# Kernel optimization log

Hardware: AMD Instinct MI355X
Metric: run time of the kernel (lower is better)

## Reference

```python
import jax, jax.numpy as jnp
import numpy as np

N_NODES, N_EDGES, F_IN, HID, N_CLASSES = 50000, 800000, 128, 128, 10
HEADS, D_HEAD, N_GRAPHS, N_CONV = 4, 32, 256, 3
BN_EPS = 1e-5
NEG_SLOPE = 0.2


def batchnorm(x, g, b):
    # training-mode BN: batch mean / biased variance over dim 0
    m = x.mean(axis=0)
    v = x.var(axis=0)
    return (x - m) * jax.lax.rsqrt(v + BN_EPS) * g + b


def segment_softmax(logits, seg, n):
    # numerically stable softmax over edges grouped by destination node
    m = jax.ops.segment_max(logits, seg, num_segments=n)
    e = jnp.exp(logits - m[seg])
    s = jax.ops.segment_sum(e, seg, num_segments=n)
    return e / (s[seg] + 1e-16)


def gat_conv(x, src, dst, W, a_src, a_dst, bias):
    # PyG GATConv (concat=True), eval mode (no attention dropout)
    n = x.shape[0]
    h = (x @ W).reshape(n, HEADS, D_HEAD)                 # [N,H,Dh]
    al_s = jnp.einsum('nhd,hd->nh', h, a_src)             # alpha from source
    al_d = jnp.einsum('nhd,hd->nh', h, a_dst)             # alpha from dest
    logits = jax.nn.leaky_relu(al_s[src] + al_d[dst], NEG_SLOPE)   # [E,H]
    alpha = segment_softmax(logits, dst, n)                # softmax over incoming edges
    msg = h[src] * alpha[:, :, None]                       # [E,H,Dh]
    out = jax.ops.segment_sum(msg, dst, num_segments=n)    # [N,H,Dh]
    return out.reshape(n, HEADS * D_HEAD) + bias


def setup_inputs() -> dict:
    key = jax.random.key(0)
    ks = jax.random.split(key, 12)
    s = 0.05
    inp = {
        'x': jax.random.normal(ks[0], (N_NODES, F_IN), dtype=jnp.float32),
        'edge_index': jax.random.randint(ks[1], (2, N_EDGES), 0, N_NODES, dtype=jnp.int32),
        'batch': jnp.sort(jax.random.randint(ks[2], (N_NODES,), 0, N_GRAPHS, dtype=jnp.int32)),
        # GCNConv(gfn=True): plain weight, no bias used
        'w_feat': s * jax.random.normal(ks[3], (F_IN, HID), dtype=jnp.float32),
        'bnf_g': jnp.ones((F_IN,), jnp.float32),
        'bnf_b': jnp.full((F_IN,), 1e-4, jnp.float32),
        'bnc_g': jnp.ones((N_CONV, HID), jnp.float32),
        'bnc_b': jnp.full((N_CONV, HID), 1e-4, jnp.float32),
        'gat_w': s * jax.random.normal(ks[4], (N_CONV, HID, HID), dtype=jnp.float32),
        'gat_asrc': s * jax.random.normal(ks[5], (N_CONV, HEADS, D_HEAD), dtype=jnp.float32),
        'gat_adst': s * jax.random.normal(ks[6], (N_CONV, HEADS, D_HEAD), dtype=jnp.float32),
        'gat_b': jnp.zeros((N_CONV, HID), jnp.float32),
        'bnfc_g': jnp.ones((HID,), jnp.float32),
        'bnfc_b': jnp.full((HID,), 1e-4, jnp.float32),
        'lin_w': s * jax.random.normal(ks[7], (HID, HID), dtype=jnp.float32),
        'lin_b': jnp.zeros((HID,), jnp.float32),
        'bnh_g': jnp.ones((HID,), jnp.float32),
        'bnh_b': jnp.full((HID,), 1e-4, jnp.float32),
        'cls_w': s * jax.random.normal(ks[8], (HID, N_CLASSES), dtype=jnp.float32),
        'cls_b': jnp.zeros((N_CLASSES,), jnp.float32),
    }
    return inp


def reference(x, edge_index, batch, w_feat, bnf_g, bnf_b, bnc_g, bnc_b,
              gat_w, gat_asrc, gat_adst, gat_b, bnfc_g, bnfc_b,
              lin_w, lin_b, bnh_g, bnh_b, cls_w, cls_b):
    n = x.shape[0]
    loops = jnp.arange(n, dtype=edge_index.dtype)
    src = jnp.concatenate([edge_index[0], loops])   # self-loops (PyG GATConv default)
    dst = jnp.concatenate([edge_index[1], loops])

    h = jax.nn.relu(batchnorm(x, bnf_g, bnf_b) @ w_feat)   # bn_feat + gfn GCNConv + relu
    for i in range(N_CONV):
        h = batchnorm(h, bnc_g[i], bnc_b[i])
        h = jax.nn.relu(gat_conv(h, src, dst, gat_w[i], gat_asrc[i], gat_adst[i], gat_b[i]))

    g = jax.ops.segment_sum(h, batch, num_segments=N_GRAPHS)   # global_add_pool [G,HID]
    g = jax.nn.relu(batchnorm(g, bnfc_g, bnfc_b) @ lin_w + lin_b)
    g = batchnorm(g, bnh_g, bnh_b)
    # dropout inactive in eval mode
    return jax.nn.log_softmax(g @ cls_w + cls_b, axis=-1)
```

## Files before the change

kernel.cpp:

```cpp
#include <hip/hip_runtime.h>
#include <math.h>

#define N_NODES 50000
#define N_EDGES 800000
#define NGRAPHS 256
#define NCONV 3
#define SCAT_CHUNK 2048
#define DMAX 64

typedef _Float16 h4 __attribute__((ext_vector_type(4)));
typedef _Float16 h8 __attribute__((ext_vector_type(8)));
typedef float f32x4 __attribute__((ext_vector_type(4)));

static inline int divup(int a, int b) { return (a + b - 1) / b; }

#define SB_CONV 0
#define SB_H1 2048
#define SB_H2 2304
#define SB_X 2560

__global__ void init_kernel(float* __restrict__ SB, int* __restrict__ cursor,
                            int* __restrict__ col, int n) {
    int i = blockIdx.x * blockDim.x + threadIdx.x;
    if (i < 2816) SB[i] = 0.f;
    if (i < n) {
        cursor[i] = 1;
        col[(size_t)i * DMAX] = i;
    }
}

__global__ __launch_bounds__(256) void scatter_edges_xcd(const int* __restrict__ src,
                                                         const int* __restrict__ dst,
                                                         int* __restrict__ cursor,
                                                         int* __restrict__ col, int E) {
    int slice = blockIdx.x & 7;
    int base = (blockIdx.x >> 3) * SCAT_CHUNK;
    int lim = min(base + SCAT_CHUNK, E);
    int lo = slice * (N_NODES / 8);
    int hi = lo + (N_NODES / 8);
    for (int i = base + threadIdx.x; i < lim; i += 256) {
        int d = dst[i];
        if (d >= lo && d < hi) {
            int p = atomicAdd(&cursor[d], 1);
            if (p < DMAX) col[(size_t)d * DMAX + p] = src[i];
        }
    }
}

__global__ __launch_bounds__(256) void cast_stats(const float* __restrict__ x,
                                                  _Float16* __restrict__ y, int n,
                                                  float* __restrict__ sums) {
    __shared__ float S[16][128], S2[16][128];
    int tid = threadIdx.x;
    int c8 = (tid & 15) * 8;
    int rg = tid >> 4;
    float s[8] = {}, s2[8] = {};
    for (int r = blockIdx.x * 16 + rg; r < n; r += gridDim.x * 16) {
        const float4* p = (const float4*)&x[(size_t)r * 128 + c8];
        float4 v0 = p[0], v1 = p[1];
        float f[8] = {v0.x, v0.y, v0.z, v0.w, v1.x, v1.y, v1.z, v1.w};
        h8 o;
#pragma unroll
        for (int i = 0; i < 8; ++i) {
            o[i] = (_Float16)f[i];
            s[i] += f[i];
            s2[i] += f[i] * f[i];
        }
        *(h8*)&y[(size_t)r * 128 + c8] = o;
    }
#pragma unroll
    for (int i = 0; i < 8; ++i) { S[rg][c8 + i] = s[i]; S2[rg][c8 + i] = s2[i]; }
    __syncthreads();
    if (tid < 128) {
        float a = 0.f, b = 0.f;
#pragma unroll
        for (int k = 0; k < 16; ++k) { a += S[k][tid]; b += S2[k][tid]; }
        atomicAdd(&sums[tid], a);
        atomicAdd(&sums[128 + tid], b);
    }
}

__global__ __launch_bounds__(256) void colstats_h(const _Float16* __restrict__ x, int n,
                                                  float* __restrict__ sums) {
    __shared__ float S[16][128], S2[16][128];
    int tid = threadIdx.x;
    int c8 = (tid & 15) * 8;
    int rg = tid >> 4;
    float s[8] = {}, s2[8] = {};
    for (int r = blockIdx.x * 16 + rg; r < n; r += gridDim.x * 16) {
        h8 v = *(const h8*)&x[(size_t)r * 128 + c8];
#pragma unroll
        for (int i = 0; i < 8; ++i) {
            float f = (float)v[i];
            s[i] += f;
            s2[i] += f * f;
        }
    }
#pragma unroll
    for (int i = 0; i < 8; ++i) { S[rg][c8 + i] = s[i]; S2[rg][c8 + i] = s2[i]; }
    __syncthreads();
    if (tid < 128) {
        float a = 0.f, b = 0.f;
#pragma unroll
        for (int k = 0; k < 16; ++k) { a += S[k][tid]; b += S2[k][tid]; }
        atomicAdd(&sums[tid], a);
        atomicAdd(&sums[128 + tid], b);
    }
}

__global__ __launch_bounds__(256) void colstats_small16(const float* __restrict__ x, int rows,
                                                        float* __restrict__ sums) {
    __shared__ float S[16][128], S2[16][128];
    int tid = threadIdx.x;
    int c8 = (tid & 15) * 8;
    int rg = tid >> 4;
    float s[8] = {}, s2[8] = {};
    for (int r = blockIdx.x * 16 + rg; r < rows; r += gridDim.x * 16) {
        const float4* p = (const float4*)&x[(size_t)r * 128 + c8];
        float4 v0 = p[0], v1 = p[1];
        float f[8] = {v0.x, v0.y, v0.z, v0.w, v1.x, v1.y, v1.z, v1.w};
#pragma unroll
        for (int i = 0; i < 8; ++i) { s[i] += f[i]; s2[i] += f[i] * f[i]; }
    }
#pragma unroll
    for (int i = 0; i < 8; ++i) { S[rg][c8 + i] = s[i]; S2[rg][c8 + i] = s2[i]; }
    __syncthreads();
    if (tid < 128) {
        float a = 0.f, b = 0.f;
#pragma unroll
        for (int k = 0; k < 16; ++k) { a += S[k][tid]; b += S2[k][tid]; }
        atomicAdd(&sums[tid], a);
        atomicAdd(&sums[128 + tid], b);
    }
}

__global__ __launch_bounds__(128) void fold_t(const float* __restrict__ sums, int nsl,
                                              float inv_n,
                                              const float* __restrict__ gamma,
                                              const float* __restrict__ beta,
                                              const float* __restrict__ W,
                                              _Float16* __restrict__ WTh, float* __restrict__ bp) {
    int j = blockIdx.x, k = threadIdx.x;
    float s1 = 0.f, s2v = 0.f;
    for (int s = 0; s < nsl; ++s) { s1 += sums[s * 256 + k]; s2v += sums[s * 256 + 128 + k]; }
    float mean = s1 * inv_n;
    float var = s2v * inv_n - mean * mean;
    float sc = gamma[k] * rsqrtf(var + 1e-5f);
    float t = beta[k] - mean * sc;
    float w = W[k * 128 + j];
    WTh[j * 128 + k] = (_Float16)(sc * w);
    float pb = t * w;
    for (int off = 1; off < 64; off <<= 1) pb += __shfl_xor(pb, off, 64);
    __shared__ float r2[2];
    if ((k & 63) == 0) r2[k >> 6] = pb;
    __syncthreads();
    if (k == 0) bp[j] = r2[0] + r2[1];
}

__global__ __launch_bounds__(256) void gemm_mfma(const _Float16* __restrict__ Ah,
                                                 const _Float16* __restrict__ WTh,
                                                 const float* __restrict__ bp,
                                                 _Float16* __restrict__ outh, int n, int relu,
                                                 const float* __restrict__ asrc,
                                                 const float* __restrict__ adst,
                                                 float* __restrict__ als,
                                                 float* __restrict__ ald,
                                                 float* __restrict__ stats8,
                                                 float* __restrict__ sums_zero) {
    __shared__ _Float16 Wl[128 * 136];
    __shared__ float SSm[4 * 128], SS2m[4 * 128];
    int tid = threadIdx.x;
    if (sums_zero && blockIdx.x < 8) sums_zero[blockIdx.x * 256 + tid] = 0.f;
    for (int i = tid; i < 2048; i += 256) {
        int r = i >> 4, s = i & 15;
        *(h8*)&Wl[r * 136 + s * 8] = *(const h8*)&WTh[r * 128 + s * 8];
    }
    __syncthreads();
    int lane = tid & 63, wid = tid >> 6;
    int m = lane & 15, quad = lane >> 4;
    int rbase = blockIdx.x * 64 + wid * 16;
    bool act = rbase < n;
    const bool do_al = (asrc != nullptr);
    const bool do_st = (stats8 != nullptr);
    float st[8] = {}, s2t[8] = {};
    float ps[4][4] = {}, pd[4][4] = {};

    if (act) {
        const _Float16* arow = Ah + (size_t)(rbase + m) * 128 + quad * 8;
        h8 af0 = *(const h8*)(arow);
        h8 af1 = *(const h8*)(arow + 32);
        h8 af2 = *(const h8*)(arow + 64);
        h8 af3 = *(const h8*)(arow + 96);
#pragma unroll
        for (int t = 0; t < 8; ++t) {
            const _Float16* wrow = &Wl[(t * 16 + m) * 136 + quad * 8];
            f32x4 acc = {0.f, 0.f, 0.f, 0.f};
            acc = __builtin_amdgcn_mfma_f32_16x16x32_f16(af0, *(const h8*)(wrow), acc, 0, 0, 0);
            acc = __builtin_amdgcn_mfma_f32_16x16x32_f16(af1, *(const h8*)(wrow + 32), acc, 0, 0, 0);
            acc = __builtin_amdgcn_mfma_f32_16x16x32_f16(af2, *(const h8*)(wrow + 64), acc, 0, 0, 0);
            acc = __builtin_amdgcn_mfma_f32_16x16x32_f16(af3, *(const h8*)(wrow + 96), acc, 0, 0, 0);
            int j = t * 16 + m;
            float bj = bp[j];
            float avs = 0.f, avd = 0.f;
            if (do_al) { avs = asrc[j]; avd = adst[j]; }
            int hh = t >> 1;
#pragma unroll
            for (int r = 0; r < 4; ++r) {
                float o = acc[r] + bj;
                if (do_al) {
                    ps[r][hh] += o * avs;
                    pd[r][hh] += o * avd;
                }
                float v = relu ? fmaxf(o, 0.f) : o;
                _Float16 hv16 = (_Float16)v;
                int row = rbase + quad * 4 + r;
                outh[(size_t)row * 128 + j] = hv16;
                if (do_st) {
                    float fv = (float)hv16;
                    st[t] += fv;
                    s2t[t] += fv * fv;
                }
            }
        }
        if (do_al) {
#pragma unroll
            for (int r = 0; r < 4; ++r) {
#pragma unroll
                for (int hh = 0; hh < 4; ++hh) {
                    float v = ps[r][hh];
                    v += __shfl_xor(v, 1, 64); v += __shfl_xor(v, 2, 64);
                    v += __shfl_xor(v, 4, 64); v += __shfl_xor(v, 8, 64);
                    float w = pd[r][hh];
                    w += __shfl_xor(w, 1, 64); w += __shfl_xor(w, 2, 64);
                    w += __shfl_xor(w, 4, 64); w += __shfl_xor(w, 8, 64);
                    if (m == 0) {
                        int row = rbase + quad * 4 + r;
                        als[row * 4 + hh] = v;
                        ald[row * 4 + hh] = w;
                    }
                }
            }
        }
    }
    if (do_st) {
#pragma unroll
        for (int t = 0; t < 8; ++t) {
            st[t] += __shfl_xor(st[t], 16, 64);  st[t] += __shfl_xor(st[t], 32, 64);
            s2t[t] += __shfl_xor(s2t[t], 16, 64); s2t[t] += __shfl_xor(s2t[t], 32, 64);
        }
        if (quad == 0) {
#pragma unroll
            for (int t = 0; t < 8; ++t) {
                SSm[wid * 128 + t * 16 + m] = st[t];
                SS2m[wid * 128 + t * 16 + m] = s2t[t];
            }
        }
        __syncthreads();
        int c = tid & 127, which = tid >> 7;
        const float* A = which ? SS2m : SSm;
        float tot = A[c] + A[128 + c] + A[256 + c] + A[384 + c];
        atomicAdd(&stats8[(blockIdx.x & 7) * 256 + which * 128 + c], tot);
    }
}

__device__ __forceinline__ float leaky(float x) { return fmaxf(x, 0.2f * x); }

__global__ __launch_bounds__(256) void gat_aggregate(const _Float16* __restrict__ hp,
                                                     const float* __restrict__ al_s,
                                                     const float* __restrict__ al_d,
                                                     const int* __restrict__ cnt_arr,
                                                     const int* __restrict__ col,
                                                     const float* __restrict__ bias,
                                                     _Float16* __restrict__ h_out,
                                                     float* __restrict__ g_zero, int n) {
    int tid = threadIdx.x;
    if (blockIdx.x < 128) g_zero[blockIdx.x * 256 + tid] = 0.f;
    int lane = tid & 63, wid = tid >> 6;
    int node = blockIdx.x * 4 + wid;
    int beg = node * DMAX;
    int end = beg + min(cnt_arr[node], DMAX);
    int q = lane >> 4, l4 = lane & 15;
    int head = l4 >> 2;
    int f0 = l4 * 8;
    float adh = al_d[node * 4 + head];
    float ch = leaky(adh);
    const _Float16* hpf = hp + f0;
    int last = end - 1;
    float ws = 0.f;
    float a0 = 0.f, a1 = 0.f, a2 = 0.f, a3 = 0.f, a4 = 0.f, a5 = 0.f, a6 = 0.f, a7 = 0.f;
    for (int e = beg + q; e < end; e += 16) {
        int e1 = e + 4, e2 = e + 8, e3 = e + 12;
        bool v1 = e1 < end, v2 = e2 < end, v3 = e3 < end;
        unsigned s0 = (unsigned)col[e];
        unsigned s1 = (unsigned)col[v1 ? e1 : last];
        unsigned s2 = (unsigned)col[v2 ? e2 : last];
        unsigned s3 = (unsigned)col[v3 ? e3 : last];
        float as0 = al_s[s0 * 4 + head];
        float as1 = al_s[s1 * 4 + head];
        float as2 = al_s[s2 * 4 + head];
        float as3 = al_s[s3 * 4 + head];
        h8 hv0 = *(const h8*)(hpf + (size_t)s0 * 128);
        h8 hv1 = *(const h8*)(hpf + (size_t)s1 * 128);
        h8 hv2 = *(const h8*)(hpf + (size_t)s2 * 128);
        h8 hv3 = *(const h8*)(hpf + (size_t)s3 * 128);
        float w0 = __expf(fminf(leaky(as0 + adh) - ch, 10.f));
        float w1 = v1 ? __expf(fminf(leaky(as1 + adh) - ch, 10.f)) : 0.f;
        float w2 = v2 ? __expf(fminf(leaky(as2 + adh) - ch, 10.f)) : 0.f;
        float w3 = v3 ? __expf(fminf(leaky(as3 + adh) - ch, 10.f)) : 0.f;
        ws += (w0 + w1) + (w2 + w3);
        a0 += (float)hv0[0] * w0 + (float)hv1[0] * w1 + (float)hv2[0] * w2 + (float)hv3[0] * w3;
        a1 += (float)hv0[1] * w0 + (float)hv1[1] * w1 + (float)hv2[1] * w2 + (float)hv3[1] * w3;
        a2 += (float)hv0[2] * w0 + (float)hv1[2] * w1 + (float)hv2[2] * w2 + (float)hv3[2] * w3;
        a3 += (float)hv0[3] * w0 + (float)hv1[3] * w1 + (float)hv2[3] * w2 + (float)hv3[3] * w3;
        a4 += (float)hv0[4] * w0 + (float)hv1[4] * w1 + (float)hv2[4] * w2 + (float)hv3[4] * w3;
        a5 += (float)hv0[5] * w0 + (float)hv1[5] * w1 + (float)hv2[5] * w2 + (float)hv3[5] * w3;
        a6 += (float)hv0[6] * w0 + (float)hv1[6] * w1 + (float)hv2[6] * w2 + (float)hv3[6] * w3;
        a7 += (float)hv0[7] * w0 + (float)hv1[7] * w1 + (float)hv2[7] * w2 + (float)hv3[7] * w3;
    }
#pragma unroll
    for (int off = 16; off <= 32; off <<= 1) {
        ws += __shfl_xor(ws, off, 64);
        a0 += __shfl_xor(a0, off, 64); a1 += __shfl_xor(a1, off, 64);
        a2 += __shfl_xor(a2, off, 64); a3 += __shfl_xor(a3, off, 64);
        a4 += __shfl_xor(a4, off, 64); a5 += __shfl_xor(a5, off, 64);
        a6 += __shfl_xor(a6, off, 64); a7 += __shfl_xor(a7, off, 64);
    }
    if (q == 0) {
        float inv = 1.f / (ws + 1e-16f);
        float4 b0 = *(const float4*)&bias[f0];
        float4 b1 = *(const float4*)&bias[f0 + 4];
        h8 ov;
        ov[0] = (_Float16)fmaxf(a0 * inv + b0.x, 0.f);
        ov[1] = (_Float16)fmaxf(a1 * inv + b0.y, 0.f);
        ov[2] = (_Float16)fmaxf(a2 * inv + b0.z, 0.f);
        ov[3] = (_Float16)fmaxf(a3 * inv + b0.w, 0.f);
        ov[4] = (_Float16)fmaxf(a4 * inv + b1.x, 0.f);
        ov[5] = (_Float16)fmaxf(a5 * inv + b1.y, 0.f);
        ov[6] = (_Float16)fmaxf(a6 * inv + b1.z, 0.f);
        ov[7] = (_Float16)fmaxf(a7 * inv + b1.w, 0.f);
        *(h8*)&h_out[(size_t)node * 128 + f0] = ov;
    }
}

__global__ void pool_kernel(const _Float16* __restrict__ h, const int* __restrict__ batch,
                            float* __restrict__ g, int n, int chunk) {
    int f = threadIdx.x;
    int a = blockIdx.x * chunk;
    if (a >= n) return;
    int b = min(n, a + chunk);
    float acc = 0.f;
    int cur = batch[a];
    for (int i = a; i < b; ++i) {
        int bi = batch[i];
        if (bi != cur) {
            atomicAdd(&g[cur * 128 + f], acc);
            acc = 0.f;
            cur = bi;
        }
        acc += (float)h[(size_t)i * 128 + f];
    }
    atomicAdd(&g[cur * 128 + f], acc);
}

__global__ __launch_bounds__(256) void gemm128_bn(const float* __restrict__ A,
                                                  const float* __restrict__ W,
                                                  const float* __restrict__ bias,
                                                  const float* __restrict__ stats, float inv_n,
                                                  const float* __restrict__ gamma,
                                                  const float* __restrict__ beta,
                                                  float* __restrict__ out, int n) {
    __shared__ float Wl[128 * 128];
    __shared__ float hT[128 * 32];
    __shared__ float sS[128], tS[128];
    int tid = threadIdx.x;
    for (int i = tid; i < 4096; i += 256) {
        ((float4*)Wl)[i] = ((const float4*)W)[i];
    }
    if (tid < 128) {
        float m = stats[tid] * inv_n;
        float var = stats[128 + tid] * inv_n - m * m;
        float sc = gamma[tid] * rsqrtf(var + 1e-5f);
        sS[tid] = sc;
        tS[tid] = beta[tid] - m * sc;
    }
    __syncthreads();
    int base = blockIdx.x * 32;
    for (int pass = 0; pass < 4; ++pass) {
        int r = (tid >> 5) + pass * 8;
        int c4 = tid & 31;
        int row = base + r;
        float4 v = (row < n) ? ((const float4*)(A + (size_t)row * 128))[c4]
                             : make_float4(0.f, 0.f, 0.f, 0.f);
        int c0 = c4 * 4;
        hT[(c0 + 0) * 32 + r] = v.x * sS[c0 + 0] + tS[c0 + 0];
        hT[(c0 + 1) * 32 + r] = v.y * sS[c0 + 1] + tS[c0 + 1];
        hT[(c0 + 2) * 32 + r] = v.z * sS[c0 + 2] + tS[c0 + 2];
        hT[(c0 + 3) * 32 + r] = v.w * sS[c0 + 3] + tS[c0 + 3];
    }
    __syncthreads();
    int tx = tid & 31, ty = tid >> 5;
    int j0 = tx * 4, r0 = ty * 4;
    float acc[4][4] = {};
#pragma unroll 8
    for (int k = 0; k < 128; ++k) {
        float4 a = *(const float4*)&hT[k * 32 + r0];
        float4 w = *(const float4*)&Wl[k * 128 + j0];
        acc[0][0] += a.x * w.x; acc[0][1] += a.x * w.y; acc[0][2] += a.x * w.z; acc[0][3] += a.x * w.w;
        acc[1][0] += a.y * w.x; acc[1][1] += a.y * w.y; acc[1][2] += a.y * w.z; acc[1][3] += a.y * w.w;
        acc[2][0] += a.z * w.x; acc[2][1] += a.z * w.y; acc[2][2] += a.z * w.z; acc[2][3] += a.z * w.w;
        acc[3][0] += a.w * w.x; acc[3][1] += a.w * w.y; acc[3][2] += a.w * w.z; acc[3][3] += a.w * w.w;
    }
    float4 bb = *(const float4*)&bias[j0];
    for (int i2 = 0; i2 < 4; ++i2) {
        int row = base + r0 + i2;
        if (row < n) {
            float4 o = make_float4(fmaxf(acc[i2][0] + bb.x, 0.f), fmaxf(acc[i2][1] + bb.y, 0.f),
                                   fmaxf(acc[i2][2] + bb.z, 0.f), fmaxf(acc[i2][3] + bb.w, 0.f));
            *(float4*)&out[(size_t)row * 128 + j0] = o;
        }
    }
}

__global__ __launch_bounds__(64) void final_kernel(const float* __restrict__ g2,
                                                   const float* __restrict__ stats, float inv_n,
                                                   const float* __restrict__ gamma,
                                                   const float* __restrict__ beta,
                                                   const float* __restrict__ W,
                                                   const float* __restrict__ b,
                                                   float* __restrict__ out, int rows) {
    int r = blockIdx.x;
    if (r >= rows) return;
    int lane = threadIdx.x;
    float logit[10] = {};
    for (int k = lane; k < 128; k += 64) {
        float m = stats[k] * inv_n;
        float var = stats[128 + k] * inv_n - m * m;
        float sc = gamma[k] * rsqrtf(var + 1e-5f);
        float gv = (g2[r * 128 + k] - m) * sc + beta[k];
#pragma unroll
        for (int j = 0; j < 10; ++j) logit[j] += gv * W[k * 10 + j];
    }
#pragma unroll
    for (int j = 0; j < 10; ++j)
        for (int off = 1; off < 64; off <<= 1) logit[j] += __shfl_xor(logit[j], off, 64);
    if (lane == 0) {
        float m = -1e30f;
#pragma unroll
        for (int j = 0; j < 10; ++j) { logit[j] += b[j]; m = fmaxf(m, logit[j]); }
        float sum = 0.f;
#pragma unroll
        for (int j = 0; j < 10; ++j) sum += expf(logit[j] - m);
        float lse = m + logf(sum);
#pragma unroll
        for (int j = 0; j < 10; ++j) out[r * 10 + j] = logit[j] - lse;
    }
}

extern "C" void kernel_launch(void* const* d_in, const int* in_sizes, int n_in,
                              void* d_out, int out_size, void* d_ws, size_t ws_size,
                              hipStream_t stream) {
    const float* x      = (const float*)d_in[0];
    const int*   ei     = (const int*)d_in[1];
    const int*   batch  = (const int*)d_in[2];
    const float* w_feat = (const float*)d_in[3];
    const float* bnf_g  = (const float*)d_in[4];
    const float* bnf_b  = (const float*)d_in[5];
    const float* bnc_g  = (const float*)d_in[6];
    const float* bnc_b  = (const float*)d_in[7];
    const float* gat_w  = (const float*)d_in[8];
    const float* gat_as = (const float*)d_in[9];
    const float* gat_ad = (const float*)d_in[10];
    const float* gat_b  = (const float*)d_in[11];
    const float* bnfc_g = (const float*)d_in[12];
    const float* bnfc_b = (const float*)d_in[13];
    const float* lin_w  = (const float*)d_in[14];
    const float* lin_b  = (const float*)d_in[15];
    const float* bnh_g  = (const float*)d_in[16];
    const float* bnh_b  = (const float*)d_in[17];
    const float* cls_w  = (const float*)d_in[18];
    const float* cls_b  = (const float*)d_in[19];
    float* out = (float*)d_out;

    char* ws = (char*)d_ws;
    size_t off = 0;
    auto alloc = [&](size_t bytes) -> void* {
        void* p = ws + off;
        off = (off + bytes + 255) & ~(size_t)255;
        return p;
    };
    _Float16* xh   = (_Float16*)alloc((size_t)N_NODES * 128 * 2);
    _Float16* h    = (_Float16*)alloc((size_t)N_NODES * 128 * 2);
    _Float16* hp   = (_Float16*)alloc((size_t)N_NODES * 128 * 2);
    float*    als  = (float*)alloc((size_t)N_NODES * 4 * 4);
    float*    ald  = (float*)alloc((size_t)N_NODES * 4 * 4);
    int*      curs = (int*)alloc((size_t)N_NODES * 4);
    int*      col  = (int*)alloc((size_t)N_NODES * DMAX * 4);
    float*    SB   = (float*)alloc(2816 * 4);
    _Float16* WTh  = (_Float16*)alloc(128 * 128 * 2);
    float*    bp   = (float*)alloc(128 * 4);
    float*    g    = (float*)alloc(NGRAPHS * 128 * 4);
    float*    g2   = (float*)alloc(NGRAPHS * 128 * 4);

    const int* esrc = ei;
    const int* edst = ei + N_EDGES;

    init_kernel<<<divup(N_NODES, 256), 256, 0, stream>>>(SB, curs, col, N_NODES);

    cast_stats<<<256, 256, 0, stream>>>(x, xh, N_NODES, SB + SB_X);
    scatter_edges_xcd<<<divup(N_EDGES, SCAT_CHUNK) * 8, 256, 0, stream>>>(esrc, edst, curs, col, N_EDGES);

    fold_t<<<128, 128, 0, stream>>>(SB + SB_X, 1, 1.f / N_NODES, bnf_g, bnf_b, w_feat, WTh, bp);
    gemm_mfma<<<divup(N_NODES, 64), 256, 0, stream>>>(xh, WTh, bp, h, N_NODES, 1,
                                                      nullptr, nullptr, nullptr, nullptr,
                                                      SB + SB_CONV, nullptr);

    for (int i = 0; i < NCONV; ++i) {
        fold_t<<<128, 128, 0, stream>>>(SB + SB_CONV, 8, 1.f / N_NODES,
                                        bnc_g + 128 * i, bnc_b + 128 * i,
                                        gat_w + 16384 * i, WTh, bp);
        gemm_mfma<<<divup(N_NODES, 64), 256, 0, stream>>>(h, WTh, bp, hp, N_NODES, 0,
                                                          gat_as + 128 * i, gat_ad + 128 * i,
                                                          als, ald, nullptr, SB + SB_CONV);
        gat_aggregate<<<N_NODES / 4, 256, 0, stream>>>(hp, als, ald, curs, col,
                                                       gat_b + 128 * i, h, g, N_NODES);
        if (i < NCONV - 1)
            colstats_h<<<256, 256, 0, stream>>>(h, N_NODES, SB + SB_CONV);
    }

    pool_kernel<<<divup(N_NODES, 32), 128, 0, stream>>>(h, batch, g, N_NODES, 32);
    colstats_small16<<<16, 256, 0, stream>>>(g, NGRAPHS, SB + SB_H1);
    gemm128_bn<<<divup(NGRAPHS, 32), 256, 0, stream>>>(g, lin_w, lin_b, SB + SB_H1,
                                                       1.f / NGRAPHS, bnfc_g, bnfc_b, g2, NGRAPHS);
    colstats_small16<<<16, 256, 0, stream>>>(g2, NGRAPHS, SB + SB_H2);
    final_kernel<<<NGRAPHS, 64, 0, stream>>>(g2, SB + SB_H2, 1.f / NGRAPHS, bnh_g, bnh_b,
                                             cls_w, cls_b, out, NGRAPHS);
}
```

Baseline: 383.1 us.

## Fuse column stats and pooling into aggregation, merge scatter with cast

Merges the edge scatter and the input cast/stats into one launch using block-index ranges. The column statistics for batchnorm and the global add pool now run inside the GAT aggregation epilogue, using LDS and global atomics. The head-stat pass for the pooled features moves inside the small dense layer. Stats buffers are double-buffered across layers so zeroing can happen inside gemm. This removes several kernel launches and extra full passes over h, at the cost of many per-node global atomics for pooling and LDS atomics in the aggregation.

```diff
diff --git a/kernel.cpp b/kernel.cpp
--- a/kernel.cpp
+++ b/kernel.cpp
@@ -14,48 +14,53 @@
 
 static inline int divup(int a, int b) { return (a + b - 1) / b; }
 
-#define SB_CONV 0
-#define SB_H1 2048
-#define SB_H2 2304
-#define SB_X 2560
+#define SB_CONV0 0
+#define SB_CONV1 2048
+#define SB_H2 4096
+#define SB_X 4352
+#define SB_TOT 4608
+
+#define NSCAT_BLOCKS 3128
 
 __global__ void init_kernel(float* __restrict__ SB, int* __restrict__ cursor,
                             int* __restrict__ col, int n) {
     int i = blockIdx.x * blockDim.x + threadIdx.x;
-    if (i < 2816) SB[i] = 0.f;
+    if (i < SB_TOT) SB[i] = 0.f;
     if (i < n) {
         cursor[i] = 1;
         col[(size_t)i * DMAX] = i;
     }
 }
 
-__global__ __launch_bounds__(256) void scatter_edges_xcd(const int* __restrict__ src,
-                                                         const int* __restrict__ dst,
-                                                         int* __restrict__ cursor,
-                                                         int* __restrict__ col, int E) {
-    int slice = blockIdx.x & 7;
-    int base = (blockIdx.x >> 3) * SCAT_CHUNK;
-    int lim = min(base + SCAT_CHUNK, E);
-    int lo = slice * (N_NODES / 8);
-    int hi = lo + (N_NODES / 8);
-    for (int i = base + threadIdx.x; i < lim; i += 256) {
-        int d = dst[i];
-        if (d >= lo && d < hi) {
-            int p = atomicAdd(&cursor[d], 1);
-            if (p < DMAX) col[(size_t)d * DMAX + p] = src[i];
-        }
-    }
-}
-
-__global__ __launch_bounds__(256) void cast_stats(const float* __restrict__ x,
-                                                  _Float16* __restrict__ y, int n,
-                                                  float* __restrict__ sums) {
+__global__ __launch_bounds__(256) void scatter_cast(const int* __restrict__ src,
+                                                    const int* __restrict__ dst,
+                                                    int* __restrict__ cursor,
+                                                    int* __restrict__ col, int E,
+                                                    const float* __restrict__ x,
+                                                    _Float16* __restrict__ y, int n,
+                                                    float* __restrict__ sums) {
+    if ((int)blockIdx.x < NSCAT_BLOCKS) {
+        int slice = blockIdx.x & 7;
+        int base = (blockIdx.x >> 3) * SCAT_CHUNK;
+        int lim = min(base + SCAT_CHUNK, E);
+        int lo = slice * (N_NODES / 8);
+        int hi = lo + (N_NODES / 8);
+        for (int i = base + threadIdx.x; i < lim; i += 256) {
+            int d = dst[i];
+            if (d >= lo && d < hi) {
+                int p = atomicAdd(&cursor[d], 1);
+                if (p < DMAX) col[(size_t)d * DMAX + p] = src[i];
+            }
+        }
+        return;
+    }
     __shared__ float S[16][128], S2[16][128];
+    int bid = blockIdx.x - NSCAT_BLOCKS;
     int tid = threadIdx.x;
     int c8 = (tid & 15) * 8;
     int rg = tid >> 4;
     float s[8] = {}, s2[8] = {};
-    for (int r = blockIdx.x * 16 + rg; r < n; r += gridDim.x * 16) {
+    for (int r = bid * 16 + rg; r < n; r += 256 * 16) {
         const float4* p = (const float4*)&x[(size_t)r * 128 + c8];
         float4 v0 = p[0], v1 = p[1];
         float f[8] = {v0.x, v0.y, v0.z, v0.w, v1.x, v1.y, v1.z, v1.w};
@@ -67,60 +72,6 @@
             s2[i] += f[i] * f[i];
         }
         *(h8*)&y[(size_t)r * 128 + c8] = o;
-    }
-#pragma unroll
-    for (int i = 0; i < 8; ++i) { S[rg][c8 + i] = s[i]; S2[rg][c8 + i] = s2[i]; }
-    __syncthreads();
-    if (tid < 128) {
-        float a = 0.f, b = 0.f;
-#pragma unroll
-        for (int k = 0; k < 16; ++k) { a += S[k][tid]; b += S2[k][tid]; }
-        atomicAdd(&sums[tid], a);
-        atomicAdd(&sums[128 + tid], b);
-    }
-}
-
-__global__ __launch_bounds__(256) void colstats_h(const _Float16* __restrict__ x, int n,
-                                                  float* __restrict__ sums) {
-    __shared__ float S[16][128], S2[16][128];
-    int tid = threadIdx.x;
-    int c8 = (tid & 15) * 8;
-    int rg = tid >> 4;
-    float s[8] = {}, s2[8] = {};
-    for (int r = blockIdx.x * 16 + rg; r < n; r += gridDim.x * 16) {
-        h8 v = *(const h8*)&x[(size_t)r * 128 + c8];
-#pragma unroll
-        for (int i = 0; i < 8; ++i) {
-            float f = (float)v[i];
-            s[i] += f;
-            s2[i] += f * f;
-        }
-    }
-#pragma unroll
-    for (int i = 0; i < 8; ++i) { S[rg][c8 + i] = s[i]; S2[rg][c8 + i] = s2[i]; }
-    __syncthreads();
-    if (tid < 128) {
-        float a = 0.f, b = 0.f;
-#pragma unroll
-        for (int k = 0; k < 16; ++k) { a += S[k][tid]; b += S2[k][tid]; }
-        atomicAdd(&sums[tid], a);
-        atomicAdd(&sums[128 + tid], b);
-    }
-}
-
-__global__ __launch_bounds__(256) void colstats_small16(const float* __restrict__ x, int rows,
-                                                        float* __restrict__ sums) {
-    __shared__ float S[16][128], S2[16][128];
-    int tid = threadIdx.x;
-    int c8 = (tid & 15) * 8;
-    int rg = tid >> 4;
-    float s[8] = {}, s2[8] = {};
-    for (int r = blockIdx.x * 16 + rg; r < rows; r += gridDim.x * 16) {
-        const float4* p = (const float4*)&x[(size_t)r * 128 + c8];
-        float4 v0 = p[0], v1 = p[1];
-        float f[8] = {v0.x, v0.y, v0.z, v0.w, v1.x, v1.y, v1.z, v1.w};
-#pragma unroll
-        for (int i = 0; i < 8; ++i) { s[i] += f[i]; s2[i] += f[i] * f[i]; }
     }
 #pragma unroll
     for (int i = 0; i < 8; ++i) { S[rg][c8 + i] = s[i]; S2[rg][c8 + i] = s2[i]; }
@@ -166,11 +117,13 @@
                                                  float* __restrict__ als,
                                                  float* __restrict__ ald,
                                                  float* __restrict__ stats8,
-                                                 float* __restrict__ sums_zero) {
+                                                 float* __restrict__ sums_zero,
+                                                 float* __restrict__ g_zero) {
     __shared__ _Float16 Wl[128 * 136];
     __shared__ float SSm[4 * 128], SS2m[4 * 128];
     int tid = threadIdx.x;
     if (sums_zero && blockIdx.x < 8) sums_zero[blockIdx.x * 256 + tid] = 0.f;
+    if (g_zero && blockIdx.x < 128) g_zero[blockIdx.x * 256 + tid] = 0.f;
     for (int i = tid; i < 2048; i += 256) {
         int r = i >> 4, s = i & 15;
         *(h8*)&Wl[r * 136 + s * 8] = *(const h8*)&WTh[r * 128 + s * 8];
@@ -272,9 +225,16 @@
                                                      const int* __restrict__ col,
                                                      const float* __restrict__ bias,
                                                      _Float16* __restrict__ h_out,
-                                                     float* __restrict__ g_zero, int n) {
+                                                     float* __restrict__ stats8,
+                                                     const int* __restrict__ batch,
+                                                     float* __restrict__ gpool, int n) {
+    __shared__ float Sl[256];
     int tid = threadIdx.x;
-    if (blockIdx.x < 128) g_zero[blockIdx.x * 256 + tid] = 0.f;
+    const bool do_st = (stats8 != nullptr);
+    if (do_st) {
+        Sl[tid] = 0.f;
+        __syncthreads();
+    }
     int lane = tid & 63, wid = tid >> 6;
     int node = blockIdx.x * 4 + wid;
     int beg = node * DMAX;
@@ -339,46 +299,64 @@
         ov[6] = (_Float16)fmaxf(a6 * inv + b1.z, 0.f);
         ov[7] = (_Float16)fmaxf(a7 * inv + b1.w, 0.f);
         *(h8*)&h_out[(size_t)node * 128 + f0] = ov;
-    }
-}
-
-__global__ void pool_kernel(const _Float16* __restrict__ h, const int* __restrict__ batch,
-                            float* __restrict__ g, int n, int chunk) {
-    int f = threadIdx.x;
-    int a = blockIdx.x * chunk;
-    if (a >= n) return;
-    int b = min(n, a + chunk);
-    float acc = 0.f;
-    int cur = batch[a];
-    for (int i = a; i < b; ++i) {
-        int bi = batch[i];
-        if (bi != cur) {
-            atomicAdd(&g[cur * 128 + f], acc);
-            acc = 0.f;
-            cur = bi;
-        }
-        acc += (float)h[(size_t)i * 128 + f];
-    }
-    atomicAdd(&g[cur * 128 + f], acc);
+        if (do_st) {
+#pragma unroll
+            for (int i = 0; i < 8; ++i) {
+                float fv = (float)ov[i];
+                atomicAdd(&Sl[f0 + i], fv);
+                atomicAdd(&Sl[128 + f0 + i], fv * fv);
+            }
+        }
+        if (batch) {
+            int bi = batch[node];
+            float* gr = gpool + (size_t)bi * 128 + f0;
+#pragma unroll
+            for (int i = 0; i < 8; ++i) atomicAdd(&gr[i], (float)ov[i]);
+        }
+    }
+    if (do_st) {
+        __syncthreads();
+        atomicAdd(&stats8[(blockIdx.x & 7) * 256 + tid], Sl[tid]);
+    }
 }
 
 __global__ __launch_bounds__(256) void gemm128_bn(const float* __restrict__ A,
                                                   const float* __restrict__ W,
                                                   const float* __restrict__ bias,
-                                                  const float* __restrict__ stats, float inv_n,
+                                                  float inv_n,
                                                   const float* __restrict__ gamma,
                                                   const float* __restrict__ beta,
-                                                  float* __restrict__ out, int n) {
+                                                  float* __restrict__ out,
+                                                  float* __restrict__ outstats, int n) {
     __shared__ float Wl[128 * 128];
     __shared__ float hT[128 * 32];
+    __shared__ float S[16][128], S2[16][128];
     __shared__ float sS[128], tS[128];
     int tid = threadIdx.x;
     for (int i = tid; i < 4096; i += 256) {
         ((float4*)Wl)[i] = ((const float4*)W)[i];
     }
+    {
+        int c8 = (tid & 15) * 8;
+        int rg = tid >> 4;
+        float s[8] = {}, s2[8] = {};
+        for (int r = rg; r < n; r += 16) {
+            const float4* p = (const float4*)&A[(size_t)r * 128 + c8];
+            float4 v0 = p[0], v1 = p[1];
+            float f[8] = {v0.x, v0.y, v0.z, v0.w, v1.x, v1.y, v1.z, v1.w};
+#pragma unroll
+            for (int i = 0; i < 8; ++i) { s[i] += f[i]; s2[i] += f[i] * f[i]; }
+        }
+#pragma unroll
+        for (int i = 0; i < 8; ++i) { S[rg][c8 + i] = s[i]; S2[rg][c8 + i] = s2[i]; }
+    }
+    __syncthreads();
     if (tid < 128) {
-        float m = stats[tid] * inv_n;
-        float var = stats[128 + tid] * inv_n - m * m;
+        float a = 0.f, b2 = 0.f;
+#pragma unroll
+        for (int k = 0; k < 16; ++k) { a += S[k][tid]; b2 += S2[k][tid]; }
+        float m = a * inv_n;
+        float var = b2 * inv_n - m * m;
         float sc = gamma[tid] * rsqrtf(var + 1e-5f);
         sS[tid] = sc;
         tS[tid] = beta[tid] - m * sc;
@@ -411,13 +389,23 @@
         acc[3][0] += a.w * w.x; acc[3][1] += a.w * w.y; acc[3][2] += a.w * w.z; acc[3][3] += a.w * w.w;
     }
     float4 bb = *(const float4*)&bias[j0];
+    float csum[4] = {}, csq[4] = {};
     for (int i2 = 0; i2 < 4; ++i2) {
         int row = base + r0 + i2;
         if (row < n) {
-            float4 o = make_float4(fmaxf(acc[i2][0] + bb.x, 0.f), fmaxf(acc[i2][1] + bb.y, 0.f),
-                                   fmaxf(acc[i2][2] + bb.z, 0.f), fmaxf(acc[i2][3] + bb.w, 0.f));
-            *(float4*)&out[(size_t)row * 128 + j0] = o;
-        }
+            float o0 = fmaxf(acc[i2][0] + bb.x, 0.f);
+            float o1 = fmaxf(acc[i2][1] + bb.y, 0.f);
+            float o2 = fmaxf(acc[i2][2] + bb.z, 0.f);
+            float o3 = fmaxf(acc[i2][3] + bb.w, 0.f);
+            *(float4*)&out[(size_t)row * 128 + j0] = make_float4(o0, o1, o2, o3);
+            csum[0] += o0; csum[1] += o1; csum[2] += o2; csum[3] += o3;
+            csq[0] += o0 * o0; csq[1] += o1 * o1; csq[2] += o2 * o2; csq[3] += o3 * o3;
+        }
+    }
+#pragma unroll
+    for (int c = 0; c < 4; ++c) {
+        atomicAdd(&outstats[j0 + c], csum[c]);
+        atomicAdd(&outstats[128 + j0 + c], csq[c]);
     }
 }
 
@@ -495,7 +483,7 @@
     float*    ald  = (float*)alloc((size_t)N_NODES * 4 * 4);
     int*      curs = (int*)alloc((size_t)N_NODES * 4);
     int*      col  = (int*)alloc((size_t)N_NODES * DMAX * 4);
-    float*    SB   = (float*)alloc(2816 * 4);
+    float*    SB   = (float*)alloc(SB_TOT * 4);
     _Float16* WTh  = (_Float16*)alloc(128 * 128 * 2);
     float*    bp   = (float*)alloc(128 * 4);
     float*    g    = (float*)alloc(NGRAPHS * 128 * 4);
@@ -506,32 +494,33 @@
 
     init_kernel<<<divup(N_NODES, 256), 256, 0, stream>>>(SB, curs, col, N_NODES);
 
-    cast_stats<<<256, 256, 0, stream>>>(x, xh, N_NODES, SB + SB_X);
-    scatter_edges_xcd<<<divup(N_EDGES, SCAT_CHUNK) * 8, 256, 0, stream>>>(esrc, edst, curs, col, N_EDGES);
+    scatter_cast<<<NSCAT_BLOCKS + 256, 256, 0, stream>>>(esrc, edst, curs, col, N_EDGES,
+                                                         x, xh, N_NODES, SB + SB_X);
 
     fold_t<<<128, 128, 0, stream>>>(SB + SB_X, 1, 1.f / N_NODES, bnf_g, bnf_b, w_feat, WTh, bp);
     gemm_mfma<<<divup(N_NODES, 64), 256, 0, stream>>>(xh, WTh, bp, h, N_NODES, 1,
                                                       nullptr, nullptr, nullptr, nullptr,
-                                                      SB + SB_CONV, nullptr);
+                                                      SB + SB_CONV0, nullptr, nullptr);
 
     for (int i = 0; i < NCONV; ++i) {
-        fold_t<<<128, 128, 0, stream>>>(SB + SB_CONV, 8, 1.f / N_NODES,
+        const float* foldsrc = (i == 1) ? SB + SB_CONV1 : SB + SB_CONV0;
+        fold_t<<<128, 128, 0, stream>>>(foldsrc, 8, 1.f / N_NODES,
                                         bnc_g + 128 * i, bnc_b + 128 * i,
                                         gat_w + 16384 * i, WTh, bp);
+        float* sz = (i == 1) ? SB + SB_CONV0 : nullptr;
+        float* gz = (i == 2) ? g : nullptr;
         gemm_mfma<<<divup(N_NODES, 64), 256, 0, stream>>>(h, WTh, bp, hp, N_NODES, 0,
                                                           gat_as + 128 * i, gat_ad + 128 * i,
-                                                          als, ald, nullptr, SB + SB_CONV);
+                                                          als, ald, nullptr, sz, gz);
+        float* stats_dst = (i == 0) ? SB + SB_CONV1 : (i == 1) ? SB + SB_CONV0 : nullptr;
         gat_aggregate<<<N_NODES / 4, 256, 0, stream>>>(hp, als, ald, curs, col,
-                                                       gat_b + 128 * i, h, g, N_NODES);
-        if (i < NCONV - 1)
-            colstats_h<<<256, 256, 0, stream>>>(h, N_NODES, SB + SB_CONV);
-    }
-
-    pool_kernel<<<divup(N_NODES, 32), 128, 0, stream>>>(h, batch, g, N_NODES, 32);
-    colstats_small16<<<16, 256, 0, stream>>>(g, NGRAPHS, SB + SB_H1);
-    gemm128_bn<<<divup(NGRAPHS, 32), 256, 0, stream>>>(g, lin_w, lin_b, SB + SB_H1,
-                                                       1.f / NGRAPHS, bnfc_g, bnfc_b, g2, NGRAPHS);
-    colstats_small16<<<16, 256, 0, stream>>>(g2, NGRAPHS, SB + SB_H2);
+                                                       gat_b + 128 * i, h, stats_dst,
+                                                       (i == 2) ? batch : nullptr,
+                                                       (i == 2) ? g : nullptr, N_NODES);
+    }
+
+    gemm128_bn<<<divup(NGRAPHS, 32), 256, 0, stream>>>(g, lin_w, lin_b, 1.f / NGRAPHS,
+                                                       bnfc_g, bnfc_b, g2, SB + SB_H2, NGRAPHS);
     final_kernel<<<NGRAPHS, 64, 0, stream>>>(g2, SB + SB_H2, 1.f / NGRAPHS, bnh_g, bnh_b,
                                              cls_w, cls_b, out, NGRAPHS);
 }
```

After: 725.9 us. +89.5%, slower.
